# Performance work log

Measured on AMD Instinct MI355X. Metric: run time of the kernel, lower is better.

The kernel has to match this reference:

```python
import jax, jax.numpy as jnp
import numpy as np

B, T, F, D, H, L = 4, 1024, 128, 512, 8, 4
DFF = 4 * D
NE, MD = 16, 20
HD = D // H
SCALE = 1.0 / HD ** 0.5


def _ln(x, w, b):
    m = jnp.mean(x, axis=-1, keepdims=True)
    v = jnp.mean((x - m) ** 2, axis=-1, keepdims=True)
    return (x - m) * jax.lax.rsqrt(v + 1e-5) * w + b


def setup_inputs() -> dict:
    key = jax.random.key(0)
    ks = jax.random.split(key, 16)
    rn = lambda k, shape: jax.random.normal(k, shape, jnp.float32) * 0.02
    return {
        'node_features': jax.random.normal(ks[0], (B, T, F), jnp.float32),
        'centrality': jax.random.uniform(ks[1], (B, T), jnp.float32),
        'edge_types': jax.random.randint(ks[2], (B, T, T), 0, NE),
        'sp_dist': jax.random.randint(ks[3], (B, T, T), 0, MD + 1),
        'node_W': rn(ks[4], (F, D)), 'node_b': jnp.zeros((D,), jnp.float32),
        'cent_W': rn(ks[5], (D,)), 'cent_b': jnp.zeros((D,), jnp.float32),
        'edge_emb': rn(ks[6], (NE, H)), 'dist_emb': rn(ks[7], (MD + 1, H)),
        'ln1_w': jnp.ones((L, D), jnp.float32), 'ln1_b': jnp.zeros((L, D), jnp.float32),
        'q_W': rn(ks[8], (L, D, D)), 'q_b': jnp.zeros((L, D), jnp.float32),
        'k_W': rn(ks[9], (L, D, D)), 'k_b': jnp.zeros((L, D), jnp.float32),
        'v_W': rn(ks[10], (L, D, D)), 'v_b': jnp.zeros((L, D), jnp.float32),
        'o_W': rn(ks[11], (L, D, D)), 'o_b': jnp.zeros((L, D), jnp.float32),
        'ln2_w': jnp.ones((L, D), jnp.float32), 'ln2_b': jnp.zeros((L, D), jnp.float32),
        'f1_W': rn(ks[12], (L, D, DFF)), 'f1_b': jnp.zeros((L, DFF), jnp.float32),
        'f2_W': rn(ks[13], (L, DFF, D)), 'f2_b': jnp.zeros((L, D), jnp.float32),
    }


def _forward(node_features, centrality, edge_types, sp_dist,
             node_W, node_b, cent_W, cent_b, edge_emb, dist_emb,
             ln1_w, ln1_b, q_W, q_b, k_W, k_b, v_W, v_b, o_W, o_b,
             ln2_w, ln2_b, f1_W, f1_b, f2_W, f2_b):
    # node embedding + centrality encoding
    h = node_features @ node_W + node_b                      # [B,T,D]
    h = h + centrality[..., None] * cent_W + cent_b          # Linear(1,D)
    # Graphormer attention bias: [B,T,T,H] -> [B,H,T,T]
    sp = jnp.clip(sp_dist, 0, MD)
    attn_bias = (edge_emb[edge_types] + dist_emb[sp]).transpose(0, 3, 1, 2)

    def step(h, p):
        l1w, l1b, qW, qb, kW, kb, vW, vb, oW, ob, l2w, l2b, w1, b1, w2, b2 = p
        x = _ln(h, l1w, l1b)
        q = (x @ qW + qb).reshape(B, T, H, HD)
        k = (x @ kW + kb).reshape(B, T, H, HD)
        v = (x @ vW + vb).reshape(B, T, H, HD)
        scores = jnp.einsum('bihd,bjhd->bhij', q, k) * SCALE + attn_bias
        attn = jax.nn.softmax(scores, axis=-1)
        o = jnp.einsum('bhij,bjhd->bihd', attn, v).reshape(B, T, D)
        h = h + (o @ oW + ob)                                # dropout in eval mode
        x2 = _ln(h, l2w, l2b)
        h = h + (jax.nn.silu(x2 @ w1 + b1) @ w2 + b2)
        return h, None

    layer_params = (ln1_w, ln1_b, q_W, q_b, k_W, k_b, v_W, v_b, o_W, o_b,
                    ln2_w, ln2_b, f1_W, f1_b, f2_W, f2_b)
    h, _ = jax.lax.scan(step, h, layer_params)
    return h


def reference(node_features, centrality, edge_types, sp_dist,
              node_W, node_b, cent_W, cent_b, edge_emb, dist_emb,
              ln1_w, ln1_b, q_W, q_b, k_W, k_b, v_W, v_b, o_W, o_b,
              ln2_w, ln2_b, f1_W, f1_b, f2_W, f2_b):
    return _forward(node_features, centrality, edge_types, sp_dist,
                    node_W, node_b, cent_W, cent_b, edge_emb, dist_emb,
                    ln1_w, ln1_b, q_W, q_b, k_W, k_b, v_W, v_b, o_W, o_b,
                    ln2_w, ln2_b, f1_W, f1_b, f2_W, f2_b)
```

## Files before the change

kernel.cpp:

```cpp
#include <hip/hip_runtime.h>
#include <cstddef>
#include <cstdint>

#define B_    4
#define T_    1024
#define F_    128
#define D_    512
#define H_    8
#define L_    4
#define DFF_  2048
#define HD_   64
#define SCALE_ 0.125f
#define LOG2E_ 1.4426950408889634f
#define CL2E_  (SCALE_ * LOG2E_)

typedef __attribute__((ext_vector_type(8))) short bf16x8;
typedef __attribute__((ext_vector_type(4))) float f32x4;

#define AS1(p) ((const __attribute__((address_space(1))) void*)(p))
#define AS3(p) ((__attribute__((address_space(3))) void*)(p))

__device__ __forceinline__ short f2bf(float f) {
    unsigned u = __float_as_uint(f);
    u += 0x7FFFu + ((u >> 16) & 1u);
    return (short)(u >> 16);
}
__device__ __forceinline__ float bf2f(short s) {
    return __uint_as_float(((unsigned)(unsigned short)s) << 16);
}

__global__ __launch_bounds__(256) void ln_k(
    const float* __restrict__ X, const float* __restrict__ w,
    const float* __restrict__ b, short* __restrict__ Y)
{
    const int row = blockIdx.x;
    const int tid = threadIdx.x;
    const float* xr = X + (size_t)row * D_;
    const float v0 = xr[tid];
    const float v1 = xr[tid + 256];
    float s  = v0 + v1;
    float s2 = v0 * v0 + v1 * v1;
#pragma unroll
    for (int off = 1; off < 64; off <<= 1) {
        s  += __shfl_xor(s,  off);
        s2 += __shfl_xor(s2, off);
    }
    __shared__ float ss[4], ss2[4];
    if ((tid & 63) == 0) { ss[tid >> 6] = s; ss2[tid >> 6] = s2; }
    __syncthreads();
    s  = ss[0]  + ss[1]  + ss[2]  + ss[3];
    s2 = ss2[0] + ss2[1] + ss2[2] + ss2[3];
    const float mean = s * (1.f / D_);
    const float var  = s2 * (1.f / D_) - mean * mean;
    const float r    = rsqrtf(var + 1e-5f);
    short* yr = Y + (size_t)row * D_;
    yr[tid]       = f2bf((v0 - mean) * r * w[tid]       + b[tid]);
    yr[tid + 256] = f2bf((v1 - mean) * r * w[tid + 256] + b[tid + 256]);
}

__global__ __launch_bounds__(256) void transpose_all_k(
    const float* __restrict__ qW, const float* __restrict__ kW,
    const float* __restrict__ vW, const float* __restrict__ oW,
    const float* __restrict__ f1W, const float* __restrict__ f2W,
    const float* __restrict__ nW,
    short* __restrict__ WqkvT, short* __restrict__ WoT,
    short* __restrict__ Wf1T, short* __restrict__ Wf2T,
    short* __restrict__ nWt)
{
    const int id = blockIdx.y;
    const float* src; short* dst; int K, N;
    if (id < 12) {
        const int l = id / 3, which = id % 3;
        const float* s3 = (which == 0) ? qW : (which == 1) ? kW : vW;
        src = s3 + (size_t)l * D_ * D_;
        dst = WqkvT + ((size_t)l * 3 + which) * D_ * D_;
        K = D_; N = D_;
    } else if (id < 16) {
        const int l = id - 12;
        src = oW + (size_t)l * D_ * D_;  dst = WoT + (size_t)l * D_ * D_;
        K = D_; N = D_;
    } else if (id < 20) {
        const int l = id - 16;
        src = f1W + (size_t)l * D_ * DFF_;  dst = Wf1T + (size_t)l * DFF_ * D_;
        K = D_; N = DFF_;
    } else if (id < 24) {
        const int l = id - 20;
        src = f2W + (size_t)l * DFF_ * D_;  dst = Wf2T + (size_t)l * D_ * DFF_;
        K = DFF_; N = D_;
    } else {
        src = nW; dst = nWt; K = F_; N = D_;
    }
    const int ntiles = (K >> 5) * (N >> 5);
    if ((int)blockIdx.x >= ntiles) return;
    const int nt = N >> 5;
    const int k0 = (blockIdx.x / nt) << 5, n0 = (blockIdx.x % nt) << 5;

    __shared__ float t[32][33];
    const int c = threadIdx.x, r0 = threadIdx.y;
#pragma unroll
    for (int i = 0; i < 32; i += 8)
        t[r0 + i][c] = src[(size_t)(k0 + r0 + i) * N + n0 + c];
    __syncthreads();
#pragma unroll
    for (int i = 0; i < 32; i += 8)
        dst[(size_t)(n0 + r0 + i) * K + k0 + c] = f2bf(t[c][r0 + i]);
}

__global__ __launch_bounds__(256) void prep_k(
    const int* __restrict__ et, const int* __restrict__ sp,
    const float* __restrict__ ee, const float* __restrict__ de,
    unsigned char* __restrict__ biasT8,
    const float* __restrict__ nf, short* __restrict__ nfb,
    const float* __restrict__ qb, const float* __restrict__ kb,
    const float* __restrict__ vb, float* __restrict__ biasf)
{
    const int bid = blockIdx.x;
    const int tid = threadIdx.x;
    if (bid >= 4096) {
        if (bid < 4608) {
            const int i = (((bid - 4096) << 8) + tid) << 2;
            const float4 v = *(const float4*)(nf + i);
            *(short4*)(nfb + i) =
                make_short4(f2bf(v.x), f2bf(v.y), f2bf(v.z), f2bf(v.w));
        } else {
            const int i = ((bid - 4608) << 8) + tid;
            const int l = i / 1536, c = i % 1536;
            float v;
            if (c < 512)       v = qb[l * 512 + c];
            else if (c < 1024) v = kb[l * 512 + c - 512];
            else               v = vb[l * 512 + c - 1024];
            biasf[i] = v;
        }
        return;
    }
    __shared__ float eeS[16][8], deS[21][8];
    if (tid < 128) eeS[tid >> 3][tid & 7] = ee[tid];
    for (int t = tid; t < 168; t += 256)
        deS[t >> 3][t & 7] = de[t];
    __syncthreads();
    const int gid = bid * 256 + tid;
    const int j4  = (gid & 255) << 2;
    const int bi  = gid >> 8;
    const size_t base = (size_t)bi * T_ + j4;
    const int4 e = *(const int4*)(et + base);
    const int4 s = *(const int4*)(sp + base);
    const int b = bi >> 10, i = bi & 1023;
    const int ex[4] = {e.x, e.y, e.z, e.w};
    const int sx[4] = {min(s.x, 20), min(s.y, 20), min(s.z, 20), min(s.w, 20)};
#pragma unroll
    for (int h = 0; h < 8; ++h) {
        uchar4 o;
        float v;
        v = (eeS[ex[0]][h] + deS[sx[0]][h]) * LOG2E_ + 0.5f;
        o.x = (unsigned char)(int)fminf(fmaxf(v * 255.f + 0.5f, 0.f), 255.f);
        v = (eeS[ex[1]][h] + deS[sx[1]][h]) * LOG2E_ + 0.5f;
        o.y = (unsigned char)(int)fminf(fmaxf(v * 255.f + 0.5f, 0.f), 255.f);
        v = (eeS[ex[2]][h] + deS[sx[2]][h]) * LOG2E_ + 0.5f;
        o.z = (unsigned char)(int)fminf(fmaxf(v * 255.f + 0.5f, 0.f), 255.f);
        v = (eeS[ex[3]][h] + deS[sx[3]][h]) * LOG2E_ + 0.5f;
        o.w = (unsigned char)(int)fminf(fmaxf(v * 255.f + 0.5f, 0.f), 255.f);
        *(uchar4*)(biasT8 + ((size_t)((b * H_ + h) * T_ + i)) * T_ + j4) = o;
    }
}

__global__ __launch_bounds__(256) void embed_mm_k(
    const short* __restrict__ A, const short* __restrict__ Wt,
    const float* __restrict__ nb, const float* __restrict__ cb,
    const float* __restrict__ cW, const float* __restrict__ cent,
    float* __restrict__ C)
{
    const int K = F_, N = D_;
    __shared__ short As[2][128 * 32];
    __shared__ short Bs[2][64 * 32];
    const int tid  = threadIdx.x;
    const int lane = tid & 63, wv = tid >> 6;
    const int bm = blockIdx.y << 7, bn = blockIdx.x << 6;
    const int wm = (wv & 1) << 6, wn = (wv >> 1) << 5;

    const int c0 = (wv << 6) + lane;
    const int m0 = c0 >> 2, q0 = (c0 & 3) ^ ((m0 >> 1) & 3);
    const int c1 = 256 + c0;
    const int m1 = c1 >> 2, q1 = (c1 & 3) ^ ((m1 >> 1) & 3);

    const short* gA0 = A  + (size_t)(bm + m0) * K + (q0 << 3);
    const short* gA1 = A  + (size_t)(bm + m1) * K + (q1 << 3);
    const short* gB0 = Wt + (size_t)(bn + m0) * K + (q0 << 3);

    f32x4 acc[4][2];
#pragma unroll
    for (int i = 0; i < 4; ++i)
#pragma unroll
        for (int j = 0; j < 2; ++j)
            acc[i][j] = (f32x4){0.f, 0.f, 0.f, 0.f};

    const int fm = lane & 15, fq = lane >> 4;
    int caddr[4], baddr[2];
#pragma unroll
    for (int t = 0; t < 4; ++t) {
        const int rowA = wm + (t << 4) + fm;
        caddr[t] = ((rowA << 2) + (fq ^ ((rowA >> 1) & 3))) << 3;
    }
#pragma unroll
    for (int t = 0; t < 2; ++t) {
        const int rowB = wn + (t << 4) + fm;
        baddr[t] = ((rowB << 2) + (fq ^ ((rowB >> 1) & 3))) << 3;
    }

#define EMB_STAGE(KK, BUF) do { \
    __builtin_amdgcn_global_load_lds(AS1(gA0 + (KK)), AS3(&As[BUF][(wv << 9)]),        16, 0, 0); \
    __builtin_amdgcn_global_load_lds(AS1(gA1 + (KK)), AS3(&As[BUF][2048 + (wv << 9)]), 16, 0, 0); \
    __builtin_amdgcn_global_load_lds(AS1(gB0 + (KK)), AS3(&Bs[BUF][(wv << 9)]),        16, 0, 0); \
} while (0)

    EMB_STAGE(0, 0);
    int cur = 0;
    for (int k0 = 0; k0 < K; k0 += 32) {
        __syncthreads();
        if (k0 + 32 < K) EMB_STAGE(k0 + 32, cur ^ 1);
        const short* Asc = As[cur];
        const short* Bsc = Bs[cur];
        bf16x8 af[4], bf[2];
#pragma unroll
        for (int t = 0; t < 4; ++t) af[t] = *(const bf16x8*)(Asc + caddr[t]);
#pragma unroll
        for (int t = 0; t < 2; ++t) bf[t] = *(const bf16x8*)(Bsc + baddr[t]);
#pragma unroll
        for (int i = 0; i < 4; ++i)
#pragma unroll
            for (int j = 0; j < 2; ++j)
                acc[i][j] = __builtin_amdgcn_mfma_f32_16x16x32_bf16(
                    af[i], bf[j], acc[i][j], 0, 0, 0);
        cur ^= 1;
    }
#undef EMB_STAGE

    const int col0 = bn + wn + fm;
    const int row0 = bm + wm + (fq << 2);
#pragma unroll
    for (int j = 0; j < 2; ++j) {
        const int colg = col0 + (j << 4);
        const float bb = nb[colg] + cb[colg];
        const float cw = cW[colg];
#pragma unroll
        for (int i = 0; i < 4; ++i) {
#pragma unroll
            for (int r = 0; r < 4; ++r) {
                const int rowg = row0 + (i << 4) + r;
                C[(size_t)rowg * N + colg] = acc[i][j][r] + bb + cent[rowg] * cw;
            }
        }
    }
}

template <int OUTM, int ACT, int RES>
__global__ __launch_bounds__(256) void mm_k(
    const short* __restrict__ A, const short* __restrict__ Wt,
    const float* __restrict__ bias, const float* __restrict__ R,
    void* __restrict__ Cv, int M, int N, int K)
{
    __shared__ short As[2][128 * 32];
    __shared__ short Bs[2][128 * 32];
    const int tid  = threadIdx.x;
    const int lane = tid & 63, wv = tid >> 6;
    const int bm = blockIdx.y << 7, bn = blockIdx.x << 7;
    const int wm = (wv & 1) << 6, wn = (wv >> 1) << 6;

    const int c0 = (wv << 6) + lane;
    const int m0 = c0 >> 2, q0 = (c0 & 3) ^ ((m0 >> 1) & 3);
    const int c1 = 256 + c0;
    const int m1 = c1 >> 2, q1 = (c1 & 3) ^ ((m1 >> 1) & 3);

    const short* gA0 = A  + (size_t)(bm + m0) * K + (q0 << 3);
    const short* gA1 = A  + (size_t)(bm + m1) * K + (q1 << 3);
    const short* gB0 = Wt + (size_t)(bn + m0) * K + (q0 << 3);
    const short* gB1 = Wt + (size_t)(bn + m1) * K + (q1 << 3);

    f32x4 acc[4][4];
#pragma unroll
    for (int i = 0; i < 4; ++i)
#pragma unroll
        for (int j = 0; j < 4; ++j)
            acc[i][j] = (f32x4){0.f, 0.f, 0.f, 0.f};

    const int fm = lane & 15, fq = lane >> 4;
    int caddr[4], baddr[4];
#pragma unroll
    for (int t = 0; t < 4; ++t) {
        const int rowA = wm + (t << 4) + fm;
        caddr[t] = ((rowA << 2) + (fq ^ ((rowA >> 1) & 3))) << 3;
        const int rowB = wn + (t << 4) + fm;
        baddr[t] = ((rowB << 2) + (fq ^ ((rowB >> 1) & 3))) << 3;
    }

#define MM_STAGE(KK, BUF) do { \
    __builtin_amdgcn_global_load_lds(AS1(gA0 + (KK)), AS3(&As[BUF][(wv << 9)]),        16, 0, 0); \
    __builtin_amdgcn_global_load_lds(AS1(gA1 + (KK)), AS3(&As[BUF][2048 + (wv << 9)]), 16, 0, 0); \
    __builtin_amdgcn_global_load_lds(AS1(gB0 + (KK)), AS3(&Bs[BUF][(wv << 9)]),        16, 0, 0); \
    __builtin_amdgcn_global_load_lds(AS1(gB1 + (KK)), AS3(&Bs[BUF][2048 + (wv << 9)]), 16, 0, 0); \
} while (0)

    MM_STAGE(0, 0);
    int cur = 0;
    for (int k0 = 0; k0 < K; k0 += 32) {
        __syncthreads();
        if (k0 + 32 < K) MM_STAGE(k0 + 32, cur ^ 1);
        const short* Asc = As[cur];
        const short* Bsc = Bs[cur];
        bf16x8 af[4], bf[4];
#pragma unroll
        for (int t = 0; t < 4; ++t) {
            af[t] = *(const bf16x8*)(Asc + caddr[t]);
            bf[t] = *(const bf16x8*)(Bsc + baddr[t]);
        }
#pragma unroll
        for (int i = 0; i < 4; ++i)
#pragma unroll
            for (int j = 0; j < 4; ++j)
                acc[i][j] = __builtin_amdgcn_mfma_f32_16x16x32_bf16(
                    af[i], bf[j], acc[i][j], 0, 0, 0);
        cur ^= 1;
    }
#undef MM_STAGE

    const int col0 = bn + wn + fm;
    const int row0 = bm + wm + (fq << 2);
    float* Cf = (float*)Cv;
    short* Cb = (short*)Cv;
#pragma unroll
    for (int j = 0; j < 4; ++j) {
        const int colg = col0 + (j << 4);
        const float bb = bias[colg];
#pragma unroll
        for (int i = 0; i < 4; ++i) {
#pragma unroll
            for (int r = 0; r < 4; ++r) {
                const int rowg = row0 + (i << 4) + r;
                float v = acc[i][j][r] + bb;
                if (ACT) v = v / (1.f + __expf(-v));
                const size_t off = (size_t)rowg * N + colg;
                if (RES) v += R[off];
                if (OUTM == 1) Cb[off] = f2bf(v);
                else           Cf[off] = v;
            }
        }
    }
}

__global__ __launch_bounds__(256) void qkv64_k(
    const short* __restrict__ A, const short* __restrict__ Wt,
    const float* __restrict__ bias, short* __restrict__ QKb,
    short* __restrict__ VtOut)
{
    const int K = D_;
    __shared__ short As[2][128 * 32];
    __shared__ short Bs[2][64 * 32];
    const int tid  = threadIdx.x;
    const int lane = tid & 63, wv = tid >> 6;
    const int bm = blockIdx.y << 7, bn = blockIdx.x << 6;
    const int wm = (wv & 1) << 6, wn = (wv >> 1) << 5;

    const int c0 = (wv << 6) + lane;
    const int m0 = c0 >> 2, q0 = (c0 & 3) ^ ((m0 >> 1) & 3);
    const int c1 = 256 + c0;
    const int m1 = c1 >> 2, q1 = (c1 & 3) ^ ((m1 >> 1) & 3);

    const short* gA0 = A  + (size_t)(bm + m0) * K + (q0 << 3);
    const short* gA1 = A  + (size_t)(bm + m1) * K + (q1 << 3);
    const short* gB0 = Wt + (size_t)(bn + m0) * K + (q0 << 3);

    f32x4 acc[4][2];
#pragma unroll
    for (int i = 0; i < 4; ++i)
#pragma unroll
        for (int j = 0; j < 2; ++j)
            acc[i][j] = (f32x4){0.f, 0.f, 0.f, 0.f};

    const int fm = lane & 15, fq = lane >> 4;
    int caddr[4], baddr[2];
#pragma unroll
    for (int t = 0; t < 4; ++t) {
        const int rowA = wm + (t << 4) + fm;
        caddr[t] = ((rowA << 2) + (fq ^ ((rowA >> 1) & 3))) << 3;
    }
#pragma unroll
    for (int t = 0; t < 2; ++t) {
        const int rowB = wn + (t << 4) + fm;
        baddr[t] = ((rowB << 2) + (fq ^ ((rowB >> 1) & 3))) << 3;
    }

#define QKV_STAGE(KK, BUF) do { \
    __builtin_amdgcn_global_load_lds(AS1(gA0 + (KK)), AS3(&As[BUF][(wv << 9)]),        16, 0, 0); \
    __builtin_amdgcn_global_load_lds(AS1(gA1 + (KK)), AS3(&As[BUF][2048 + (wv << 9)]), 16, 0, 0); \
    __builtin_amdgcn_global_load_lds(AS1(gB0 + (KK)), AS3(&Bs[BUF][(wv << 9)]),        16, 0, 0); \
} while (0)

    QKV_STAGE(0, 0);
    int cur = 0;
    for (int k0 = 0; k0 < K; k0 += 32) {
        __syncthreads();
        if (k0 + 32 < K) QKV_STAGE(k0 + 32, cur ^ 1);
        const short* Asc = As[cur];
        const short* Bsc = Bs[cur];
        bf16x8 af[4], bf[2];
#pragma unroll
        for (int t = 0; t < 4; ++t) af[t] = *(const bf16x8*)(Asc + caddr[t]);
#pragma unroll
        for (int t = 0; t < 2; ++t) bf[t] = *(const bf16x8*)(Bsc + baddr[t]);
#pragma unroll
        for (int i = 0; i < 4; ++i)
#pragma unroll
            for (int j = 0; j < 2; ++j)
                acc[i][j] = __builtin_amdgcn_mfma_f32_16x16x32_bf16(
                    af[i], bf[j], acc[i][j], 0, 0, 0);
        cur ^= 1;
    }
#undef QKV_STAGE

    const int col0 = bn + wn + fm;
    const int row0 = bm + wm + (fq << 2);
#pragma unroll
    for (int j = 0; j < 2; ++j) {
        const int colg = col0 + (j << 4);
        const float bb = bias[colg];
#pragma unroll
        for (int i = 0; i < 4; ++i) {
#pragma unroll
            for (int r = 0; r < 4; ++r) {
                const int rowg = row0 + (i << 4) + r;
                const float v = acc[i][j][r] + bb;
                if (colg < 1024) {
                    QKb[(size_t)rowg * 1024 + colg] = f2bf(v);
                } else {
                    const int da = colg - 1024;
                    const int hh = da >> 6, dd = da & 63;
                    const int bb2 = rowg >> 10, tt = rowg & 1023;
                    VtOut[((size_t)(bb2 * H_ + hh) * 64 + dd) * T_ + tt] = f2bf(v);
                }
            }
        }
    }
}

__global__ __launch_bounds__(256) void flash_k(
    const short* __restrict__ QKb, const short* __restrict__ Vt,
    const unsigned char* __restrict__ biasT8, short* __restrict__ OpartB,
    float* __restrict__ Lpart)
{
    const int tid = threadIdx.x;
    const int bx = blockIdx.x;
    const int it = bx >> 1, split = bx & 1;
    const int i0 = it << 6;
    const int h  = blockIdx.y;
    const int b  = blockIdx.z;
    const int lane = tid & 63, w = tid >> 6;
    const int fm = lane & 15, q = lane >> 4;

    __shared__ short Ks[2][4096];
    __shared__ short Vs[2][4096];
    __shared__ unsigned char Bsh8[2][4096];
    __shared__ short Ps[64][72];

    const short* qp = QKb + (size_t)(b * T_ + i0 + (w << 4) + fm) * 1024 + (h << 6) + (q << 3);
    const bf16x8 aq0 = *(const bf16x8*)(qp);
    const bf16x8 aq1 = *(const bf16x8*)(qp + 32);

    const int s0 = (w << 6) + lane, r0 = s0 >> 3, cc0 = (s0 & 7) ^ (r0 & 7);
    const int s1 = 256 + s0,        r1 = s1 >> 3, cc1 = (s1 & 7) ^ (r1 & 7);
    const short* gK0 = QKb + (size_t)(b * T_ + r0) * 1024 + 512 + (h << 6) + (cc0 << 3);
    const short* gK1 = QKb + (size_t)(b * T_ + r1) * 1024 + 512 + (h << 6) + (cc1 << 3);
    const short* gV0 = Vt + ((size_t)((b * H_ + h) << 6) + r0) * T_ + (cc0 << 3);
    const short* gV1 = Vt + ((size_t)((b * H_ + h) << 6) + r1) * T_ + (cc1 << 3);
    const int br = s0 >> 2, bc = (s0 & 3) ^ (br & 3);
    const unsigned char* gB0 = biasT8 +
        ((size_t)(b * H_ + h) * T_ + i0 + br) * T_ + (bc << 4);

    int fAddr[4][2];
#pragma unroll
    for (int t = 0; t < 4; ++t) {
        const int row = (t << 4) + fm;
#pragma unroll
        for (int ks = 0; ks < 2; ++ks)
            fAddr[t][ks] = (row << 6) + (((q + (ks << 2)) ^ (row & 7)) << 3);
    }

    int bAddr[4][4];
#pragma unroll
    for (int r = 0; r < 4; ++r) {
        const int rowL = (w << 4) + (q << 2) + r;
#pragma unroll
        for (int jt = 0; jt < 4; ++jt)
            bAddr[r][jt] = (rowL << 6) + (((jt ^ (rowL & 3))) << 4) + fm;
    }

    const short oneb = 0x3F80;
    const bf16x8 ones = {oneb, oneb, oneb, oneb, oneb, oneb, oneb, oneb};

    f32x4 accO[4];
#pragma unroll
    for (int dt = 0; dt < 4; ++dt) accO[dt] = (f32x4){0.f, 0.f, 0.f, 0.f};
    f32x4 accL = (f32x4){0.f, 0.f, 0.f, 0.f};

    const int irow = b * T_ + i0 + (w << 4) + (q << 2);
    short* psW = &Ps[(w << 4) + (q << 2)][fm];
    const short* psR = &Ps[(w << 4) + fm][q << 3];

#define FLASH_STAGE(J0, BUF) do { \
    __builtin_amdgcn_global_load_lds(AS1(gK0 + (size_t)(J0) * 1024), AS3(&Ks[BUF][s0 << 3]), 16, 0, 0); \
    __builtin_amdgcn_global_load_lds(AS1(gK1 + (size_t)(J0) * 1024), AS3(&Ks[BUF][s1 << 3]), 16, 0, 0); \
    __builtin_amdgcn_global_load_lds(AS1(gV0 + (J0)), AS3(&Vs[BUF][s0 << 3]), 16, 0, 0); \
    __builtin_amdgcn_global_load_lds(AS1(gV1 + (J0)), AS3(&Vs[BUF][s1 << 3]), 16, 0, 0); \
    __builtin_amdgcn_global_load_lds(AS1(gB0 + (J0)), AS3(&Bsh8[BUF][s0 << 4]), 16, 0, 0); \
} while (0)

    const int jbeg = split << 9, jend = jbeg + 512;
    FLASH_STAGE(jbeg, 0);
    int cur = 0;
    for (int j0 = jbeg; j0 < jend; j0 += 64) {
        __syncthreads();
        if (j0 + 64 < jend) FLASH_STAGE(j0 + 64, cur ^ 1);
        const short* Ksc = Ks[cur];
        const short* Vsc = Vs[cur];
        const unsigned char* Bc = Bsh8[cur];

        f32x4 s[4];
#pragma unroll
        for (int jt = 0; jt < 4; ++jt) s[jt] = (f32x4){0.f, 0.f, 0.f, 0.f};
#pragma unroll
        for (int jt = 0; jt < 4; ++jt) {
            const bf16x8 k0 = *(const bf16x8*)(Ksc + fAddr[jt][0]);
            const bf16x8 k1 = *(const bf16x8*)(Ksc + fAddr[jt][1]);
            s[jt] = __builtin_amdgcn_mfma_f32_16x16x32_bf16(aq0, k0, s[jt], 0, 0, 0);
            s[jt] = __builtin_amdgcn_mfma_f32_16x16x32_bf16(aq1, k1, s[jt], 0, 0, 0);
        }

#pragma unroll
        for (int r = 0; r < 4; ++r)
#pragma unroll
            for (int jt = 0; jt < 4; ++jt) {
                const float q8 = (float)Bc[bAddr[r][jt]];
                const float bb = fmaf(q8, 1.f / 255.f, -0.5f);
                const float p = __builtin_amdgcn_exp2f(fmaf(s[jt][r], CL2E_, bb));
                psW[(size_t)r * 72 + (jt << 4)] = f2bf(p);
            }

#pragma unroll
        for (int ks = 0; ks < 2; ++ks) {
            const bf16x8 ap = *(const bf16x8*)(psR + (ks << 5));
            accL = __builtin_amdgcn_mfma_f32_16x16x32_bf16(ap, ones, accL, 0, 0, 0);
#pragma unroll
            for (int dt = 0; dt < 4; ++dt) {
                const bf16x8 bv = *(const bf16x8*)(Vsc + fAddr[dt][ks]);
                accO[dt] = __builtin_amdgcn_mfma_f32_16x16x32_bf16(ap, bv, accO[dt], 0, 0, 0);
            }
        }
        cur ^= 1;
    }
#undef FLASH_STAGE

    short* obase = OpartB + (size_t)split * B_ * T_ * D_;
#pragma unroll
    for (int r = 0; r < 4; ++r) {
        short* op = obase + (size_t)(irow + r) * D_ + (h << 6) + fm;
#pragma unroll
        for (int dt = 0; dt < 4; ++dt)
            op[dt << 4] = f2bf(accO[dt][r]);
    }
    if (fm == 0) {
#pragma unroll
        for (int r = 0; r < 4; ++r)
            Lpart[(size_t)split * B_ * T_ * H_ + (size_t)(irow + r) * H_ + h] = accL[r];
    }
}

__global__ __launch_bounds__(256) void combine_k(
    const short* __restrict__ OpartB, const float* __restrict__ Lpart,
    short* __restrict__ Ob)
{
    const int gid = blockIdx.x * 256 + threadIdx.x;
    const int d4  = (gid & 127) << 2;
    const int row = gid >> 7;
    const int h   = d4 >> 6;
    const float l = Lpart[(size_t)row * H_ + h] +
                    Lpart[(size_t)B_ * T_ * H_ + (size_t)row * H_ + h];
    const float inv = 1.f / l;
    const size_t o = (size_t)row * D_ + d4;
    const short4 a = *(const short4*)(OpartB + o);
    const short4 c = *(const short4*)(OpartB + (size_t)B_ * T_ * D_ + o);
    short4 r = make_short4(
        f2bf((bf2f(a.x) + bf2f(c.x)) * inv), f2bf((bf2f(a.y) + bf2f(c.y)) * inv),
        f2bf((bf2f(a.z) + bf2f(c.z)) * inv), f2bf((bf2f(a.w) + bf2f(c.w)) * inv));
    *(short4*)(Ob + o) = r;
}

__global__ __launch_bounds__(256) void mm64_k(
    const short* __restrict__ A, const short* __restrict__ Wt,
    const float* __restrict__ bias, const float* __restrict__ R,
    float* __restrict__ C, int M, int N, int K)
{
    __shared__ short As[2][128 * 32];
    __shared__ short Bs[2][64 * 32];
    const int tid  = threadIdx.x;
    const int lane = tid & 63, wv = tid >> 6;
    const int bm = blockIdx.y << 7, bn = blockIdx.x << 6;
    const int wm = (wv & 1) << 6, wn = (wv >> 1) << 5;

    const int c0 = (wv << 6) + lane;
    const int m0 = c0 >> 2, q0 = (c0 & 3) ^ ((m0 >> 1) & 3);
    const int c1 = 256 + c0;
    const int m1 = c1 >> 2, q1 = (c1 & 3) ^ ((m1 >> 1) & 3);

    const short* gA0 = A  + (size_t)(bm + m0) * K + (q0 << 3);
    const short* gA1 = A  + (size_t)(bm + m1) * K + (q1 << 3);
    const short* gB0 = Wt + (size_t)(bn + m0) * K + (q0 << 3);

    f32x4 acc[4][2];
#pragma unroll
    for (int i = 0; i < 4; ++i)
#pragma unroll
        for (int j = 0; j < 2; ++j)
            acc[i][j] = (f32x4){0.f, 0.f, 0.f, 0.f};

    const int fm = lane & 15, fq = lane >> 4;
    int caddr[4], baddr[2];
#pragma unroll
    for (int t = 0; t < 4; ++t) {
        const int rowA = wm + (t << 4) + fm;
        caddr[t] = ((rowA << 2) + (fq ^ ((rowA >> 1) & 3))) << 3;
    }
#pragma unroll
    for (int t = 0; t < 2; ++t) {
        const int rowB = wn + (t << 4) + fm;
        baddr[t] = ((rowB << 2) + (fq ^ ((rowB >> 1) & 3))) << 3;
    }

#define MM64_STAGE(KK, BUF) do { \
    __builtin_amdgcn_global_load_lds(AS1(gA0 + (KK)), AS3(&As[BUF][(wv << 9)]),        16, 0, 0); \
    __builtin_amdgcn_global_load_lds(AS1(gA1 + (KK)), AS3(&As[BUF][2048 + (wv << 9)]), 16, 0, 0); \
    __builtin_amdgcn_global_load_lds(AS1(gB0 + (KK)), AS3(&Bs[BUF][(wv << 9)]),        16, 0, 0); \
} while (0)

    MM64_STAGE(0, 0);
    int cur = 0;
    for (int k0 = 0; k0 < K; k0 += 32) {
        __syncthreads();
        if (k0 + 32 < K) MM64_STAGE(k0 + 32, cur ^ 1);
        const short* Asc = As[cur];
        const short* Bsc = Bs[cur];
        bf16x8 af[4], bf[2];
#pragma unroll
        for (int t = 0; t < 4; ++t) af[t] = *(const bf16x8*)(Asc + caddr[t]);
#pragma unroll
        for (int t = 0; t < 2; ++t) bf[t] = *(const bf16x8*)(Bsc + baddr[t]);
#pragma unroll
        for (int i = 0; i < 4; ++i)
#pragma unroll
            for (int j = 0; j < 2; ++j)
                acc[i][j] = __builtin_amdgcn_mfma_f32_16x16x32_bf16(
                    af[i], bf[j], acc[i][j], 0, 0, 0);
        cur ^= 1;
    }
#undef MM64_STAGE

    const int col0 = bn + wn + fm;
    const int row0 = bm + wm + (fq << 2);
#pragma unroll
    for (int j = 0; j < 2; ++j) {
        const int colg = col0 + (j << 4);
        const float bb = bias[colg];
#pragma unroll
        for (int i = 0; i < 4; ++i) {
#pragma unroll
            for (int r = 0; r < 4; ++r) {
                const int rowg = row0 + (i << 4) + r;
                const size_t off = (size_t)rowg * N + colg;
                C[off] = acc[i][j][r] + bb + R[off];
            }
        }
    }
}

extern "C" void kernel_launch(void* const* d_in, const int* in_sizes, int n_in,
                              void* d_out, int out_size, void* d_ws, size_t ws_size,
                              hipStream_t stream)
{
    (void)in_sizes; (void)n_in; (void)out_size; (void)ws_size;

    const float* nf   = (const float*)d_in[0];
    const float* cent = (const float*)d_in[1];
    const int*   et   = (const int*)  d_in[2];
    const int*   sp   = (const int*)  d_in[3];
    const float* nW   = (const float*)d_in[4];
    const float* nb   = (const float*)d_in[5];
    const float* cW   = (const float*)d_in[6];
    const float* cb   = (const float*)d_in[7];
    const float* ee   = (const float*)d_in[8];
    const float* de   = (const float*)d_in[9];
    const float* ln1w = (const float*)d_in[10];
    const float* ln1b = (const float*)d_in[11];
    const float* qW   = (const float*)d_in[12];
    const float* qb   = (const float*)d_in[13];
    const float* kW   = (const float*)d_in[14];
    const float* kb   = (const float*)d_in[15];
    const float* vW   = (const float*)d_in[16];
    const float* vb   = (const float*)d_in[17];
    const float* oW   = (const float*)d_in[18];
    const float* ob   = (const float*)d_in[19];
    const float* ln2w = (const float*)d_in[20];
    const float* ln2b = (const float*)d_in[21];
    const float* f1W  = (const float*)d_in[22];
    const float* f1b  = (const float*)d_in[23];
    const float* f2W  = (const float*)d_in[24];
    const float* f2b  = (const float*)d_in[25];

    const int M = B_ * T_;
    char* p = (char*)d_ws;
    float* Hbuf  = (float*)p;  p += (size_t)M * D_ * 4;
    short* QKb   = (short*)p;  p += (size_t)M * 1024 * 2;
    short* Vt    = (short*)p;  p += (size_t)B_ * H_ * 64 * T_ * 2;
    float* biasf = (float*)p;  p += (size_t)L_ * 3 * D_ * 4;
    short* Xbuf  = (short*)p;  p += (size_t)M * D_ * 2;
    short* Ob    = (short*)p;  p += (size_t)M * D_ * 2;
    short* FF    = (short*)p;  p += (size_t)M * DFF_ * 2;
    unsigned char* biasT8 = (unsigned char*)p; p += (size_t)B_ * H_ * T_ * T_;
    short* WqkvT = (short*)p;  p += (size_t)L_ * 3 * D_ * D_ * 2;
    short* WoT   = (short*)p;  p += (size_t)L_ * D_ * D_ * 2;
    short* Wf1T  = (short*)p;  p += (size_t)L_ * DFF_ * D_ * 2;
    short* Wf2T  = (short*)p;  p += (size_t)L_ * D_ * DFF_ * 2;
    short* nfb   = (short*)p;  p += (size_t)M * F_ * 2;
    short* nWt   = (short*)p;  p += (size_t)D_ * F_ * 2;
    short* OpartB = (short*)p; p += (size_t)2 * M * D_ * 2;
    float* Lpart = (float*)p;  p += (size_t)2 * M * H_ * 4;

    float* out = (float*)d_out;

    transpose_all_k<<<dim3(1024, 25), dim3(32, 8), 0, stream>>>(
        qW, kW, vW, oW, f1W, f2W, nW, WqkvT, WoT, Wf1T, Wf2T, nWt);
    prep_k<<<dim3(4632), dim3(256), 0, stream>>>(
        et, sp, ee, de, biasT8, nf, nfb, qb, kb, vb, biasf);
    embed_mm_k<<<dim3(D_ / 64, M / 128), dim3(256), 0, stream>>>(
        nfb, nWt, nb, cb, cW, cent, Hbuf);

    const dim3 blk(256);
    const dim3 gQKV(3 * D_ / 64, M / 128);
    const dim3 gO64(D_ / 64,     M / 128);
    const dim3 gF1 (DFF_ / 128,  M / 128);
    const dim3 gAttn(2 * T_ / 64, H_, B_);
    const dim3 gCmb(M * D_ / 1024);

    for (int l = 0; l < L_; ++l) {
        const size_t bOff  = (size_t)l * D_;
        const size_t b1Off = (size_t)l * DFF_;

        ln_k<<<dim3(M), blk, 0, stream>>>(Hbuf, ln1w + bOff, ln1b + bOff, Xbuf);

        qkv64_k<<<gQKV, blk, 0, stream>>>(
            Xbuf, WqkvT + (size_t)l * 3 * D_ * D_, biasf + (size_t)l * 3 * D_,
            QKb, Vt);

        flash_k<<<gAttn, blk, 0, stream>>>(QKb, Vt, biasT8, OpartB, Lpart);
        combine_k<<<gCmb, blk, 0, stream>>>(OpartB, Lpart, Ob);

        mm64_k<<<gO64, blk, 0, stream>>>(
            Ob, WoT + (size_t)l * D_ * D_, ob + bOff, Hbuf, Hbuf, M, D_, D_);

        ln_k<<<dim3(M), blk, 0, stream>>>(Hbuf, ln2w + bOff, ln2b + bOff, Xbuf);

        mm_k<1, 1, 0><<<gF1, blk, 0, stream>>>(
            Xbuf, Wf1T + (size_t)l * DFF_ * D_, f1b + b1Off, nullptr, FF, M, DFF_, D_);

        float* cdst = (l == L_ - 1) ? out : Hbuf;
        mm64_k<<<gO64, blk, 0, stream>>>(
            FF, Wf2T + (size_t)l * D_ * DFF_, f2b + bOff, Hbuf, cdst, M, D_, DFF_);
    }
}
```

Before: 684.0 us.

## Split-K output/FFN2 GEMMs with atomic residual accumulation; single-buffer flash tiles

The O-projection and FFN2 GEMMs now split K four ways across blockIdx.z and accumulate with atomic adds straight into the residual buffer. This removes the separate residual read and gives a 4x larger grid to fill the GPU. Because the last layer now writes into the residual buffer, a final copy kernel moves it to the output. Separately, the flash kernel drops LDS double buffering for a single buffer with two barriers per tile. That lowers LDS use, which may raise occupancy, but loses load/compute overlap. Atomic float adds make the summation order nondeterministic.

```diff
diff --git a/kernel.cpp b/kernel.cpp
--- a/kernel.cpp
+++ b/kernel.cpp
@@ -455,9 +455,9 @@
     const int lane = tid & 63, w = tid >> 6;
     const int fm = lane & 15, q = lane >> 4;
 
-    __shared__ short Ks[2][4096];
-    __shared__ short Vs[2][4096];
-    __shared__ unsigned char Bsh8[2][4096];
+    __shared__ short Ks[4096];
+    __shared__ short Vs[4096];
+    __shared__ unsigned char Bsh8[4096];
     __shared__ short Ps[64][72];
 
     const short* qp = QKb + (size_t)(b * T_ + i0 + (w << 4) + fm) * 1024 + (h << 6) + (q << 3);
@@ -504,31 +504,23 @@
     short* psW = &Ps[(w << 4) + (q << 2)][fm];
     const short* psR = &Ps[(w << 4) + fm][q << 3];
 
-#define FLASH_STAGE(J0, BUF) do { \
-    __builtin_amdgcn_global_load_lds(AS1(gK0 + (size_t)(J0) * 1024), AS3(&Ks[BUF][s0 << 3]), 16, 0, 0); \
-    __builtin_amdgcn_global_load_lds(AS1(gK1 + (size_t)(J0) * 1024), AS3(&Ks[BUF][s1 << 3]), 16, 0, 0); \
-    __builtin_amdgcn_global_load_lds(AS1(gV0 + (J0)), AS3(&Vs[BUF][s0 << 3]), 16, 0, 0); \
-    __builtin_amdgcn_global_load_lds(AS1(gV1 + (J0)), AS3(&Vs[BUF][s1 << 3]), 16, 0, 0); \
-    __builtin_amdgcn_global_load_lds(AS1(gB0 + (J0)), AS3(&Bsh8[BUF][s0 << 4]), 16, 0, 0); \
-} while (0)
-
     const int jbeg = split << 9, jend = jbeg + 512;
-    FLASH_STAGE(jbeg, 0);
-    int cur = 0;
     for (int j0 = jbeg; j0 < jend; j0 += 64) {
         __syncthreads();
-        if (j0 + 64 < jend) FLASH_STAGE(j0 + 64, cur ^ 1);
-        const short* Ksc = Ks[cur];
-        const short* Vsc = Vs[cur];
-        const unsigned char* Bc = Bsh8[cur];
+        __builtin_amdgcn_global_load_lds(AS1(gK0 + (size_t)j0 * 1024), AS3(Ks + (s0 << 3)), 16, 0, 0);
+        __builtin_amdgcn_global_load_lds(AS1(gK1 + (size_t)j0 * 1024), AS3(Ks + (s1 << 3)), 16, 0, 0);
+        __builtin_amdgcn_global_load_lds(AS1(gV0 + j0), AS3(Vs + (s0 << 3)), 16, 0, 0);
+        __builtin_amdgcn_global_load_lds(AS1(gV1 + j0), AS3(Vs + (s1 << 3)), 16, 0, 0);
+        __builtin_amdgcn_global_load_lds(AS1(gB0 + j0), AS3(Bsh8 + (s0 << 4)), 16, 0, 0);
+        __syncthreads();
 
         f32x4 s[4];
 #pragma unroll
         for (int jt = 0; jt < 4; ++jt) s[jt] = (f32x4){0.f, 0.f, 0.f, 0.f};
 #pragma unroll
         for (int jt = 0; jt < 4; ++jt) {
-            const bf16x8 k0 = *(const bf16x8*)(Ksc + fAddr[jt][0]);
-            const bf16x8 k1 = *(const bf16x8*)(Ksc + fAddr[jt][1]);
+            const bf16x8 k0 = *(const bf16x8*)(Ks + fAddr[jt][0]);
+            const bf16x8 k1 = *(const bf16x8*)(Ks + fAddr[jt][1]);
             s[jt] = __builtin_amdgcn_mfma_f32_16x16x32_bf16(aq0, k0, s[jt], 0, 0, 0);
             s[jt] = __builtin_amdgcn_mfma_f32_16x16x32_bf16(aq1, k1, s[jt], 0, 0, 0);
         }
@@ -537,7 +529,7 @@
         for (int r = 0; r < 4; ++r)
 #pragma unroll
             for (int jt = 0; jt < 4; ++jt) {
-                const float q8 = (float)Bc[bAddr[r][jt]];
+                const float q8 = (float)Bsh8[bAddr[r][jt]];
                 const float bb = fmaf(q8, 1.f / 255.f, -0.5f);
                 const float p = __builtin_amdgcn_exp2f(fmaf(s[jt][r], CL2E_, bb));
                 psW[(size_t)r * 72 + (jt << 4)] = f2bf(p);
@@ -549,13 +541,11 @@
             accL = __builtin_amdgcn_mfma_f32_16x16x32_bf16(ap, ones, accL, 0, 0, 0);
 #pragma unroll
             for (int dt = 0; dt < 4; ++dt) {
-                const bf16x8 bv = *(const bf16x8*)(Vsc + fAddr[dt][ks]);
+                const bf16x8 bv = *(const bf16x8*)(Vs + fAddr[dt][ks]);
                 accO[dt] = __builtin_amdgcn_mfma_f32_16x16x32_bf16(ap, bv, accO[dt], 0, 0, 0);
             }
         }
-        cur ^= 1;
-    }
-#undef FLASH_STAGE
+    }
 
     short* obase = OpartB + (size_t)split * B_ * T_ * D_;
 #pragma unroll
@@ -592,16 +582,17 @@
     *(short4*)(Ob + o) = r;
 }
 
-__global__ __launch_bounds__(256) void mm64_k(
+__global__ __launch_bounds__(256) void mm64sk_k(
     const short* __restrict__ A, const short* __restrict__ Wt,
-    const float* __restrict__ bias, const float* __restrict__ R,
-    float* __restrict__ C, int M, int N, int K)
+    const float* __restrict__ bias, float* __restrict__ C,
+    int M, int N, int K, int KS)
 {
     __shared__ short As[2][128 * 32];
     __shared__ short Bs[2][64 * 32];
     const int tid  = threadIdx.x;
     const int lane = tid & 63, wv = tid >> 6;
     const int bm = blockIdx.y << 7, bn = blockIdx.x << 6;
+    const int ks0 = blockIdx.z * KS;
     const int wm = (wv & 1) << 6, wn = (wv >> 1) << 5;
 
     const int c0 = (wv << 6) + lane;
@@ -609,9 +600,9 @@
     const int c1 = 256 + c0;
     const int m1 = c1 >> 2, q1 = (c1 & 3) ^ ((m1 >> 1) & 3);
 
-    const short* gA0 = A  + (size_t)(bm + m0) * K + (q0 << 3);
-    const short* gA1 = A  + (size_t)(bm + m1) * K + (q1 << 3);
-    const short* gB0 = Wt + (size_t)(bn + m0) * K + (q0 << 3);
+    const short* gA0 = A  + (size_t)(bm + m0) * K + ks0 + (q0 << 3);
+    const short* gA1 = A  + (size_t)(bm + m1) * K + ks0 + (q1 << 3);
+    const short* gB0 = Wt + (size_t)(bn + m0) * K + ks0 + (q0 << 3);
 
     f32x4 acc[4][2];
 #pragma unroll
@@ -641,9 +632,9 @@
 
     MM64_STAGE(0, 0);
     int cur = 0;
-    for (int k0 = 0; k0 < K; k0 += 32) {
+    for (int k0 = 0; k0 < KS; k0 += 32) {
         __syncthreads();
-        if (k0 + 32 < K) MM64_STAGE(k0 + 32, cur ^ 1);
+        if (k0 + 32 < KS) MM64_STAGE(k0 + 32, cur ^ 1);
         const short* Asc = As[cur];
         const short* Bsc = Bs[cur];
         bf16x8 af[4], bf[2];
@@ -663,20 +654,28 @@
 
     const int col0 = bn + wn + fm;
     const int row0 = bm + wm + (fq << 2);
+    const bool addb = (blockIdx.z == 0);
 #pragma unroll
     for (int j = 0; j < 2; ++j) {
         const int colg = col0 + (j << 4);
-        const float bb = bias[colg];
+        const float bb = addb ? bias[colg] : 0.f;
 #pragma unroll
         for (int i = 0; i < 4; ++i) {
 #pragma unroll
             for (int r = 0; r < 4; ++r) {
                 const int rowg = row0 + (i << 4) + r;
                 const size_t off = (size_t)rowg * N + colg;
-                C[off] = acc[i][j][r] + bb + R[off];
+                unsafeAtomicAdd(&C[off], acc[i][j][r] + bb);
             }
         }
     }
+}
+
+__global__ __launch_bounds__(256) void copy_k(
+    const float* __restrict__ S, float* __restrict__ Dst)
+{
+    const int i = (blockIdx.x * 256 + threadIdx.x) << 2;
+    *(float4*)(Dst + i) = *(const float4*)(S + i);
 }
 
 extern "C" void kernel_launch(void* const* d_in, const int* in_sizes, int n_in,
@@ -742,7 +741,7 @@
 
     const dim3 blk(256);
     const dim3 gQKV(3 * D_ / 64, M / 128);
-    const dim3 gO64(D_ / 64,     M / 128);
+    const dim3 gO64sk(D_ / 64, M / 128, 4);
     const dim3 gF1 (DFF_ / 128,  M / 128);
     const dim3 gAttn(2 * T_ / 64, H_, B_);
     const dim3 gCmb(M * D_ / 1024);
@@ -760,16 +759,17 @@
         flash_k<<<gAttn, blk, 0, stream>>>(QKb, Vt, biasT8, OpartB, Lpart);
         combine_k<<<gCmb, blk, 0, stream>>>(OpartB, Lpart, Ob);
 
-        mm64_k<<<gO64, blk, 0, stream>>>(
-            Ob, WoT + (size_t)l * D_ * D_, ob + bOff, Hbuf, Hbuf, M, D_, D_);
+        mm64sk_k<<<gO64sk, blk, 0, stream>>>(
+            Ob, WoT + (size_t)l * D_ * D_, ob + bOff, Hbuf, M, D_, D_, D_ / 4);
 
         ln_k<<<dim3(M), blk, 0, stream>>>(Hbuf, ln2w + bOff, ln2b + bOff, Xbuf);
 
         mm_k<1, 1, 0><<<gF1, blk, 0, stream>>>(
             Xbuf, Wf1T + (size_t)l * DFF_ * D_, f1b + b1Off, nullptr, FF, M, DFF_, D_);
 
-        float* cdst = (l == L_ - 1) ? out : Hbuf;
-        mm64_k<<<gO64, blk, 0, stream>>>(
-            FF, Wf2T + (size_t)l * D_ * DFF_, f2b + bOff, Hbuf, cdst, M, D_, DFF_);
-    }
-}
+        mm64sk_k<<<gO64sk, blk, 0, stream>>>(
+            FF, Wf2T + (size_t)l * D_ * DFF_, f2b + bOff, Hbuf, M, D_, DFF_, DFF_ / 4);
+    }
+
+    copy_k<<<gCmb, blk, 0, stream>>>(Hbuf, out);
+}
```

After: 789.3 us. 15.4% more time.
